# Optimization experiments

Measured on AMD Instinct MI355X. Metric: run time of the kernel, lower is better.

Reference implementation:

```python
import jax, jax.numpy as jnp
import numpy as np

B, N, E = 256, 256, 512
ITER = 10

def setup_inputs() -> dict:
    key = jax.random.key(0)
    k1, k2, k3 = jax.random.split(key, 3)
    feats = jax.random.normal(k1, (B, N, E), dtype=jnp.float32)
    logits = jax.random.normal(k2, (B, N, 1), dtype=jnp.float32)
    # nn.Parameter initialized to zeros in the original; use small random values
    # so the CRF update is non-trivial for correctness checking.
    W = jax.random.normal(k3, (1, N, N), dtype=jnp.float32) * 0.01
    return {"feats": feats, "logits": logits, "W": W}

def reference(feats, logits, W):
    # cosine similarity between all node pairs: [B, N, N]
    feats_norm = jnp.linalg.norm(feats, axis=2, keepdims=True)          # [B,N,1]
    pairwise_norm = feats_norm @ jnp.swapaxes(feats_norm, 1, 2)         # [B,N,N]
    pairwise_dot = jnp.einsum('bne,bme->bnm', feats, feats)             # [B,N,N]
    pairwise_sim = pairwise_dot / pairwise_norm
    W_sym = (W + jnp.swapaxes(W, 1, 2)) * 0.5                           # [1,N,N]
    pairwise_potential = pairwise_sim * W_sym                           # [B,N,N]
    unary_potential = logits                                            # [B,N,1]

    def step(lg, _):
        probs = jnp.swapaxes(jax.nn.sigmoid(lg), 1, 2)                  # [B,1,N]
        # probs*P - (1-probs)*P == (2*probs - 1)*P
        e = jnp.sum((2.0 * probs - 1.0) * pairwise_potential,
                    axis=2, keepdims=True)                              # [B,N,1]
        return unary_potential + e, None

    out, _ = jax.lax.scan(step, logits, None, length=ITER)
    return out
```

## Files before the change

### kernel.cpp

```cpp
#include <hip/hip_runtime.h>
#include <hip/hip_bf16.h>
#include <math.h>

#define Bb   256
#define Nn   256
#define Ee   512
#define TKF  32
#define NCH  (Ee / TKF)
#define NITER 10

typedef __attribute__((ext_vector_type(8))) short bf16x8;
typedef __attribute__((ext_vector_type(4))) float f32x4;

typedef __attribute__((address_space(1))) const void glb_cv;
typedef __attribute__((address_space(3))) void lds_v;

#define VMCNT(n) asm volatile("s_waitcnt vmcnt(" #n ")" ::: "memory")
#define LGKM0()  asm volatile("s_waitcnt lgkmcnt(0)" ::: "memory")

static __device__ __forceinline__ unsigned short f2bf(float f) {
    __hip_bfloat16 h = __float2bfloat16(f);
    return __builtin_bit_cast(unsigned short, h);
}

static __device__ __forceinline__ bf16x8 ldfrag(const unsigned char* bt, int row, int hi) {
    const int byte = row * 64 + ((hi * 16) ^ ((row & 3) << 4));
    return *reinterpret_cast<const bf16x8*>(bt + byte);
}

__global__ __launch_bounds__(256) void wsym_k(const float* __restrict__ W,
                                              float* __restrict__ wsym) {
    const int idx = blockIdx.x * 256 + threadIdx.x;
    const int r  = idx >> 6;
    const int c0 = (idx & 63) * 4;
    const float4 a = *reinterpret_cast<const float4*>(&W[r * Nn + c0]);
    float4 o;
    o.x = 0.5f * (a.x + W[(c0 + 0) * Nn + r]);
    o.y = 0.5f * (a.y + W[(c0 + 1) * Nn + r]);
    o.z = 0.5f * (a.z + W[(c0 + 2) * Nn + r]);
    o.w = 0.5f * (a.w + W[(c0 + 3) * Nn + r]);
    *reinterpret_cast<float4*>(&wsym[r * Nn + c0]) = o;
}

template <bool USE_WS>
__global__ __launch_bounds__(512, 2) void crf_mfma(
    const float* __restrict__ feats,
    const float* __restrict__ logits,
    const float* __restrict__ W,
    const float* __restrict__ wsym,
    float* __restrict__ out)
{
    const int b    = blockIdx.x;
    const int t    = threadIdx.x;
    const int wave = t >> 6;
    const int lane = t & 63;
    const int wr   = wave >> 1;
    const int wc   = wave & 1;
    const int lo   = lane & 15;
    const int hi   = lane >> 4;

    __shared__ float fstage[2][Nn * TKF];
    __shared__ unsigned char btile[2][Nn * 64];
    __shared__ float invn[Nn];
    __shared__ float svec[Nn];
    __shared__ float uvec[Nn];
    __shared__ float lgv[Nn];
    __shared__ float part[4][Nn];

    f32x4 acc[4][8];
#pragma unroll
    for (int i = 0; i < 4; ++i)
#pragma unroll
        for (int j = 0; j < 8; ++j) acc[i][j] = (f32x4){0.f, 0.f, 0.f, 0.f};

    const float* Fb = feats + (size_t)b * Nn * Ee;

    auto stage = [&](int ch, int buf) {
#pragma unroll
        for (int i = 0; i < 4; ++i) {
            const int gbase = wave * 4 + i;
            const int row   = gbase * 8 + (lane >> 3);
            const float* src = Fb + (size_t)row * Ee + ch * TKF + (lane & 7) * 4;
            __builtin_amdgcn_global_load_lds((glb_cv*)src,
                                             (lds_v*)(&fstage[buf][gbase * 256]), 16, 0, 0);
        }
    };

    auto convert = [&](int buf) {
#pragma unroll
        for (int g = 0; g < 4; ++g) {
            const int m   = t + 512 * g;
            const int row = m >> 3;
            const int gc  = m & 7;
            const float4 v = *reinterpret_cast<const float4*>(&fstage[buf][m * 4]);
            ushort4 pk;
            pk.x = f2bf(v.x); pk.y = f2bf(v.y); pk.z = f2bf(v.z); pk.w = f2bf(v.w);
            *reinterpret_cast<ushort4*>(
                &btile[buf][row * 64 + ((gc * 8) ^ ((row & 3) << 4))]) = pk;
        }
    };

    auto mfma_step = [&](int buf) {
        const unsigned char* tb = &btile[buf][0];
        bf16x8 af[4];
#pragma unroll
        for (int rb = 0; rb < 4; ++rb)
            af[rb] = ldfrag(tb, wr * 64 + rb * 16 + lo, hi);
#pragma unroll
        for (int cg = 0; cg < 2; ++cg) {
            bf16x8 bfv[4];
#pragma unroll
            for (int cq = 0; cq < 4; ++cq)
                bfv[cq] = ldfrag(tb, wc * 128 + (cg * 4 + cq) * 16 + lo, hi);
#pragma unroll
            for (int rb = 0; rb < 4; ++rb)
#pragma unroll
                for (int cq = 0; cq < 4; ++cq)
                    acc[rb][cg * 4 + cq] = __builtin_amdgcn_mfma_f32_16x16x32_bf16(
                        af[rb], bfv[cq], acc[rb][cg * 4 + cq], 0, 0, 0);
        }
    };

    float uval = 0.f;
    if (t < Nn) uval = logits[(size_t)b * Nn + t];
    stage(0, 0);
    stage(1, 1);
    if (t < Nn) {
        uvec[t] = uval;
        lgv[t]  = uval;
    }

#pragma unroll 2
    for (int ch = 0; ch < NCH; ++ch) {
        if (ch + 1 < NCH) { VMCNT(4); } else { VMCNT(0); }
        __builtin_amdgcn_s_barrier();
        convert(ch & 1);
        LGKM0();
        __builtin_amdgcn_s_barrier();
        if (ch + 2 < NCH) stage(ch + 2, ch & 1);
        mfma_step(ch & 1);
    }

#pragma unroll
    for (int rb = 0; rb < 4; ++rb) {
        const int rowbase = wr * 64 + rb * 16;
#pragma unroll
        for (int cb = 0; cb < 8; ++cb) {
            const int colbase = wc * 128 + cb * 16;
            if (rowbase == colbase) {
#pragma unroll
                for (int r = 0; r < 4; ++r) {
                    if (hi * 4 + r == lo)
                        invn[rowbase + hi * 4 + r] = 1.0f / sqrtf(acc[rb][cb][r]);
                }
            }
        }
    }
    __syncthreads();

#pragma unroll
    for (int rb = 0; rb < 4; ++rb) {
        const int rbase = wr * 64 + rb * 16 + hi * 4;
        const float4 ir4 = *reinterpret_cast<const float4*>(&invn[rbase]);
        const float ir[4] = {ir4.x, ir4.y, ir4.z, ir4.w};
#pragma unroll
        for (int cb = 0; cb < 8; ++cb) {
            const int col = wc * 128 + cb * 16 + lo;
            const float ic = invn[col];
            if (USE_WS) {
#pragma unroll
                for (int r = 0; r < 4; ++r) {
                    const float ws = wsym[(rbase + r) * Nn + col];
                    acc[rb][cb][r] = acc[rb][cb][r] * ir[r] * ic * ws;
                }
            } else {
                const float4 wt = *reinterpret_cast<const float4*>(&W[col * Nn + rbase]);
                const float wtr[4] = {wt.x, wt.y, wt.z, wt.w};
#pragma unroll
                for (int r = 0; r < 4; ++r) {
                    const float ws = 0.5f * (W[(rbase + r) * Nn + col] + wtr[r]);
                    acc[rb][cb][r] = acc[rb][cb][r] * ir[r] * ic * ws;
                }
            }
        }
    }

    for (int itr = 0; itr < NITER; ++itr) {
        if (t < Nn) {
            const float x = lgv[t];
            svec[t] = 2.f / (1.f + __expf(-x)) - 1.f;
        }
        __syncthreads();

        float ep[8] = {0.f, 0.f, 0.f, 0.f, 0.f, 0.f, 0.f, 0.f};
#pragma unroll
        for (int rb = 0; rb < 4; ++rb) {
            const float4 s4 = *reinterpret_cast<const float4*>(
                &svec[wr * 64 + rb * 16 + hi * 4]);
#pragma unroll
            for (int cb = 0; cb < 8; ++cb)
                ep[cb] += acc[rb][cb][0] * s4.x + acc[rb][cb][1] * s4.y
                        + acc[rb][cb][2] * s4.z + acc[rb][cb][3] * s4.w;
        }
#pragma unroll
        for (int cb = 0; cb < 8; ++cb) {
            ep[cb] += __shfl_xor(ep[cb], 16);
            ep[cb] += __shfl_xor(ep[cb], 32);
        }
        if (lane < 16) {
#pragma unroll
            for (int cb = 0; cb < 8; ++cb)
                part[wr][wc * 128 + cb * 16 + lane] = ep[cb];
        }
        __syncthreads();
        if (t < Nn)
            lgv[t] = uvec[t] + part[0][t] + part[1][t] + part[2][t] + part[3][t];
    }

    if (t < Nn) out[(size_t)b * Nn + t] = lgv[t];
}

extern "C" void kernel_launch(void* const* d_in, const int* in_sizes, int n_in,
                              void* d_out, int out_size, void* d_ws, size_t ws_size,
                              hipStream_t stream) {
    const float* feats  = (const float*)d_in[0];
    const float* logits = (const float*)d_in[1];
    const float* W      = (const float*)d_in[2];
    float* out = (float*)d_out;

    if (ws_size >= (size_t)Nn * Nn * sizeof(float)) {
        float* wsym = (float*)d_ws;
        wsym_k<<<dim3(64), dim3(256), 0, stream>>>(W, wsym);
        crf_mfma<true><<<dim3(Bb), dim3(512), 0, stream>>>(feats, logits, W, wsym, out);
    } else {
        crf_mfma<false><<<dim3(Bb), dim3(512), 0, stream>>>(feats, logits, W, nullptr, out);
    }
}
```

Measured before the change: 45.69 us.

## Replace LDS fp32 staging with register prefetch and a double-buffered bf16 tile

Drops the global_load_lds fp32 staging buffer. Each thread now prefetches feature chunks into registers, converts them to bf16 and writes them straight into the swizzled bf16 tile, while the MFMAs run on the other buffer. This removes one LDS round trip and one barrier per chunk, and frees 64KB of LDS per block, which could allow more blocks per CU. In exchange it uses 32 more VGPRs for the in-flight registers, which may pressure occupancy under launch_bounds(512,2).

```diff
diff --git a/kernel.cpp b/kernel.cpp
--- a/kernel.cpp
+++ b/kernel.cpp
@@ -12,10 +12,6 @@
 typedef __attribute__((ext_vector_type(8))) short bf16x8;
 typedef __attribute__((ext_vector_type(4))) float f32x4;
 
-typedef __attribute__((address_space(1))) const void glb_cv;
-typedef __attribute__((address_space(3))) void lds_v;
-
-#define VMCNT(n) asm volatile("s_waitcnt vmcnt(" #n ")" ::: "memory")
 #define LGKM0()  asm volatile("s_waitcnt lgkmcnt(0)" ::: "memory")
 
 static __device__ __forceinline__ unsigned short f2bf(float f) {
@@ -59,7 +55,6 @@
     const int lo   = lane & 15;
     const int hi   = lane >> 4;
 
-    __shared__ float fstage[2][Nn * TKF];
     __shared__ unsigned char btile[2][Nn * 64];
     __shared__ float invn[Nn];
     __shared__ float svec[Nn];
@@ -75,30 +70,31 @@
 
     const float* Fb = feats + (size_t)b * Nn * Ee;
 
-    auto stage = [&](int ch, int buf) {
-#pragma unroll
-        for (int i = 0; i < 4; ++i) {
-            const int gbase = wave * 4 + i;
-            const int row   = gbase * 8 + (lane >> 3);
-            const float* src = Fb + (size_t)row * Ee + ch * TKF + (lane & 7) * 4;
-            __builtin_amdgcn_global_load_lds((glb_cv*)src,
-                                             (lds_v*)(&fstage[buf][gbase * 256]), 16, 0, 0);
-        }
-    };
-
-    auto convert = [&](int buf) {
-#pragma unroll
-        for (int g = 0; g < 4; ++g) {
-            const int m   = t + 512 * g;
-            const int row = m >> 3;
-            const int gc  = m & 7;
-            const float4 v = *reinterpret_cast<const float4*>(&fstage[buf][m * 4]);
-            ushort4 pk;
-            pk.x = f2bf(v.x); pk.y = f2bf(v.y); pk.z = f2bf(v.z); pk.w = f2bf(v.w);
-            *reinterpret_cast<ushort4*>(
-                &btile[buf][row * 64 + ((gc * 8) ^ ((row & 3) << 4))]) = pk;
-        }
-    };
+    const int row0 = t >> 3;
+    const int gc   = t & 7;
+
+    float4 sA[4], sB[4];
+
+#define LOADCHUNK(ch, s)                                                    \
+    {                                                                       \
+        _Pragma("unroll")                                                   \
+        for (int i = 0; i < 4; ++i)                                         \
+            s[i] = *reinterpret_cast<const float4*>(                        \
+                Fb + (size_t)(row0 + 64 * i) * Ee + (ch) * TKF + gc * 4);   \
+    }
+
+#define CVTWRITE(s, buf)                                                    \
+    {                                                                       \
+        _Pragma("unroll")                                                   \
+        for (int i = 0; i < 4; ++i) {                                       \
+            const int row = row0 + 64 * i;                                  \
+            ushort4 pk;                                                     \
+            pk.x = f2bf(s[i].x); pk.y = f2bf(s[i].y);                       \
+            pk.z = f2bf(s[i].z); pk.w = f2bf(s[i].w);                       \
+            *reinterpret_cast<ushort4*>(                                    \
+                &btile[buf][row * 64 + ((gc * 8) ^ ((row & 3) << 4))]) = pk;\
+        }                                                                   \
+    }
 
     auto mfma_step = [&](int buf) {
         const unsigned char* tb = &btile[buf][0];
@@ -123,22 +119,27 @@
 
     float uval = 0.f;
     if (t < Nn) uval = logits[(size_t)b * Nn + t];
-    stage(0, 0);
-    stage(1, 1);
+    LOADCHUNK(0, sA);
+    LOADCHUNK(1, sB);
     if (t < Nn) {
         uvec[t] = uval;
         lgv[t]  = uval;
     }
-
-#pragma unroll 2
-    for (int ch = 0; ch < NCH; ++ch) {
-        if (ch + 1 < NCH) { VMCNT(4); } else { VMCNT(0); }
-        __builtin_amdgcn_s_barrier();
-        convert(ch & 1);
+    CVTWRITE(sA, 0);
+    LGKM0();
+    __builtin_amdgcn_s_barrier();
+
+    for (int ch2 = 0; ch2 < NCH; ch2 += 2) {
+        if (ch2 + 2 < NCH) LOADCHUNK(ch2 + 2, sA);
+        CVTWRITE(sB, 1);
+        mfma_step(0);
         LGKM0();
         __builtin_amdgcn_s_barrier();
-        if (ch + 2 < NCH) stage(ch + 2, ch & 1);
-        mfma_step(ch & 1);
+        if (ch2 + 3 < NCH) LOADCHUNK(ch2 + 3, sB);
+        if (ch2 + 2 < NCH) CVTWRITE(sA, 0);
+        mfma_step(1);
+        LGKM0();
+        __builtin_amdgcn_s_barrier();
     }
 
 #pragma unroll
@@ -218,6 +219,8 @@
     }
 
     if (t < Nn) out[(size_t)b * Nn + t] = lgv[t];
+#undef LOADCHUNK
+#undef CVTWRITE
 }
 
 extern "C" void kernel_launch(void* const* d_in, const int* in_sizes, int n_in,
```

New measurement: 45.56 us. Within noise of the previous version (-0.3%).
